# Optimization experiments

Measured on AMD Instinct MI355X. Metric: run time of the kernel, lower is better.

## Reference

```python
import jax, jax.numpy as jnp
import numpy as np

DIM = 1024
TOPK = 64
PAIRS = DIM // 2  # phase_pairs default
PHASE_MIX = 0.5
GATE_THRESHOLD = 0.0
EPS = 1e-12  # F.normalize default eps


def _l2norm(v):
    # matches F.normalize(v, dim=-1): v / max(||v||, eps)
    n = jnp.linalg.norm(v, axis=-1, keepdims=True)
    return v / jnp.maximum(n, EPS)


def setup_inputs() -> dict:
    key = jax.random.key(0)
    ks = jax.random.split(key, 6)
    s = 0.02  # small init scale for weights
    return {
        "x": jax.random.normal(ks[0], (4, 4096, DIM), dtype=jnp.float32),
        "gate_W": jax.random.normal(ks[1], (DIM, DIM), dtype=jnp.float32) * s,
        "gate_b": jnp.zeros((DIM,), dtype=jnp.float32),
        "mag_W": jax.random.normal(ks[2], (DIM, DIM), dtype=jnp.float32) * s,
        "mag_b": jnp.zeros((DIM,), dtype=jnp.float32),
        "Wq": jax.random.normal(ks[3], (DIM, DIM), dtype=jnp.float32) * s,
        "Wk": jax.random.normal(ks[4], (DIM, DIM), dtype=jnp.float32) * s,
        "phase_W": jax.random.normal(ks[5], (2 * PAIRS, DIM), dtype=jnp.float32) * s,
    }


def reference(x, gate_W, gate_b, mag_W, mag_b, Wq, Wk, phase_W):
    B, S, D = x.shape
    # gated SAE-style projection (gated=True, diag=False)
    gate_pre = x @ gate_W.T + gate_b          # [B,S,D]
    mag_pre = x @ mag_W.T + mag_b             # [B,S,D]
    # hard gate with straight-through estimator
    gate_soft = jax.nn.sigmoid(gate_pre)
    gate_hard = (gate_pre > GATE_THRESHOLD).astype(x.dtype)
    gate = gate_hard + gate_soft - jax.lax.stop_gradient(gate_soft)
    mag = jax.nn.relu(mag_pre)
    # top-k scatter mask along feature dim
    idx = jax.lax.top_k(gate_pre, TOPK)[1]    # [B,S,K]
    rows = jnp.arange(B * S)[:, None]
    mask = (jnp.zeros((B * S, D), dtype=bool)
            .at[rows, idx.reshape(B * S, TOPK)].set(True)
            .reshape(B, S, D))
    gate = jnp.where(mask, gate, jnp.zeros_like(gate))
    mag = jnp.where(mask, mag, jnp.zeros_like(mag))
    xg = gate * mag
    # twist projections, L2-normalized
    q = _l2norm(xg @ Wq.T)
    k = _l2norm(xg @ Wk.T)
    # symplectic momentum map over consecutive steps
    momentum_map = q[:, 1:] * k[:, :-1] - q[:, :-1] * k[:, 1:]  # [B,S-1,D]
    twist_mag = jnp.linalg.norm(momentum_map, axis=-1, keepdims=True)
    complexity = jnp.pad(jnp.tanh(twist_mag), ((0, 0), (1, 0), (0, 0)))  # [B,S,1]
    # phase branch (phase_mix > 0)
    phase = (xg @ phase_W.T).reshape(B, S, PAIRS, 2)
    phase = _l2norm(phase)
    pp, pc = phase[:, :-1], phase[:, 1:]
    cross = pp[..., 0] * pc[..., 1] - pp[..., 1] * pc[..., 0]   # [B,S-1,P]
    dot = jnp.clip(jnp.sum(pp * pc, axis=-1), -1.0, 1.0)
    phase_delta = jnp.abs(jnp.arctan2(cross, dot)) / jnp.pi
    phase_score = jnp.pad(jnp.mean(phase_delta, axis=-1, keepdims=True),
                          ((0, 0), (1, 0), (0, 0)))             # [B,S,1]
    return (1.0 - PHASE_MIX) * complexity + PHASE_MIX * phase_score
```

## Files before the change

### kernel.cpp

```cpp
#include <hip/hip_runtime.h>
#include <math.h>

#define DIM 1024
#define ROWS 16384
#define SEQ 4096
#define MARGIN 0.006f
#define MAXC 24

typedef __bf16 v8bf __attribute__((ext_vector_type(8)));
typedef float v4f __attribute__((ext_vector_type(4)));

__device__ __forceinline__ unsigned short f2bf(float f){
  unsigned u = __float_as_uint(f);
  u = u + 0x7FFFu + ((u >> 16) & 1u);
  return (unsigned short)(u >> 16);
}
__device__ __forceinline__ float bf2f(unsigned short h){
  return __uint_as_float(((unsigned)h) << 16);
}
__device__ __forceinline__ unsigned short relu_bf(unsigned short h){
  return (h & 0x8000u) ? (unsigned short)0 : h;
}
__device__ __forceinline__ void lds_fence(){
  __asm__ volatile("s_waitcnt lgkmcnt(0)" ::: "memory");
}

__global__ __launch_bounds__(256) void cvt_k(const float* __restrict__ s,
                                             unsigned short* __restrict__ d, int n){
  int i = (blockIdx.x * 256 + threadIdx.x) * 4;
  if (i + 3 < n){
    float4 f = *(const float4*)(s + i);
    ushort4 o;
    o.x = f2bf(f.x); o.y = f2bf(f.y); o.z = f2bf(f.z); o.w = f2bf(f.w);
    *(ushort4*)(d + i) = o;
  }
}

__global__ __launch_bounds__(256) void cvt_w(
    const float* __restrict__ w0, const float* __restrict__ w1,
    const float* __restrict__ w2, const float* __restrict__ w3,
    const float* __restrict__ w4, unsigned short* __restrict__ dst){
  const float* srcs[5] = {w0, w1, w2, w3, w4};
  const float* s = srcs[blockIdx.y];
  int i = (blockIdx.x * 256 + threadIdx.x) * 4;
  float4 f = *(const float4*)(s + i);
  ushort4 o;
  o.x = f2bf(f.x); o.y = f2bf(f.y); o.z = f2bf(f.z); o.w = f2bf(f.w);
  *(ushort4*)(dst + ((size_t)blockIdx.y << 20) + i) = o;
}

__global__ __launch_bounds__(256, 4) void gemm_bt(
    const unsigned short* __restrict__ A, const unsigned short* __restrict__ B,
    const float* __restrict__ bias0, const float* __restrict__ bias1,
    void* __restrict__ C0, void* __restrict__ C1, void* __restrict__ C2,
    int bf16mask)
{
  __shared__ unsigned short lA[128 * 32];
  __shared__ unsigned short lB[128 * 32];
  const int t = threadIdx.x;
  const int lane = t & 63, wave = t >> 6;
  const int m0 = blockIdx.y * 128, n0 = blockIdx.x * 128;
  const int wm = (wave >> 1) * 64, wn = (wave & 1) * 64;
  const int ar = lane & 15, aq = lane >> 4;

  v4f acc[4][4];
#pragma unroll
  for (int i = 0; i < 4; i++)
#pragma unroll
    for (int j = 0; j < 4; j++) acc[i][j] = v4f{0.f, 0.f, 0.f, 0.f};

  for (int k0 = 0; k0 < DIM; k0 += 32){
#pragma unroll
    for (int i = 0; i < 2; i++){
      int c = (wave * 2 + i) * 64 + lane;
      int row = c >> 2, kq = c & 3;
      __builtin_amdgcn_global_load_lds(
        (const __attribute__((address_space(1))) void*)(A + (size_t)(m0 + row) * DIM + k0 + kq * 8),
        (__attribute__((address_space(3))) void*)(&lA[c * 8]), 16, 0, 0);
      __builtin_amdgcn_global_load_lds(
        (const __attribute__((address_space(1))) void*)(B + (size_t)(n0 + row) * DIM + k0 + kq * 8),
        (__attribute__((address_space(3))) void*)(&lB[c * 8]), 16, 0, 0);
    }
    __syncthreads();
    v8bf af[4], bf[4];
#pragma unroll
    for (int i = 0; i < 4; i++){
      af[i] = *(const v8bf*)&lA[(wm + i * 16 + ar) * 32 + aq * 8];
      bf[i] = *(const v8bf*)&lB[(wn + i * 16 + ar) * 32 + aq * 8];
    }
#pragma unroll
    for (int mi = 0; mi < 4; mi++)
#pragma unroll
      for (int ni = 0; ni < 4; ni++)
        acc[mi][ni] = __builtin_amdgcn_mfma_f32_16x16x32_bf16(af[mi], bf[ni], acc[mi][ni], 0, 0, 0);
    __syncthreads();
  }

  const int os = n0 >> 10;
  void* Cp = (os == 0) ? C0 : ((os == 1) ? C1 : C2);
  const float* bp = (os == 0) ? bias0 : ((os == 1) ? bias1 : nullptr);
  const bool half_out = ((bf16mask >> os) & 1) != 0;
#pragma unroll
  for (int mi = 0; mi < 4; mi++)
#pragma unroll
    for (int ni = 0; ni < 4; ni++){
      int col = (n0 + wn + ni * 16 + ar) & (DIM - 1);
      float bv = bp ? bp[col] : 0.f;
#pragma unroll
      for (int rr = 0; rr < 4; rr++){
        int rowg = m0 + wm + mi * 16 + aq * 4 + rr;
        float val = acc[mi][ni][rr] + bv;
        if (half_out) ((unsigned short*)Cp)[(size_t)rowg * DIM + col] = f2bf(val);
        else          ((float*)Cp)[(size_t)rowg * DIM + col] = val;
      }
    }
}

__global__ __launch_bounds__(256) void select_k(
  const float* __restrict__ gate_pre, const unsigned short* __restrict__ mag_pre,
  const float* __restrict__ x, const float* __restrict__ gW, const float* __restrict__ gb,
  unsigned short* __restrict__ xg)
{
  __shared__ int   s_cnt[4];
  __shared__ int   s_idx[4][MAXC];
  __shared__ float s_ex [4][MAXC];
  __shared__ int   s_res[4][MAXC];

  const int t = threadIdx.x;
  const int lane = t & 63, wave = t >> 6;
  const int r = blockIdx.x * 4 + wave;
  const size_t rb = (size_t)r * DIM;

  float vg[16], vx[16];
  unsigned short mg[16];
#pragma unroll
  for (int c = 0; c < 4; c++){
    float4 g4 = *(const float4*)(gate_pre + rb + c * 256 + lane * 4);
    float4 x4 = *(const float4*)(x        + rb + c * 256 + lane * 4);
    ushort4 m4 = *(const ushort4*)(mag_pre + rb + c * 256 + lane * 4);
    vg[c*4+0]=g4.x; vg[c*4+1]=g4.y; vg[c*4+2]=g4.z; vg[c*4+3]=g4.w;
    vx[c*4+0]=x4.x; vx[c*4+1]=x4.y; vx[c*4+2]=x4.z; vx[c*4+3]=x4.w;
    mg[c*4+0]=m4.x; mg[c*4+1]=m4.y; mg[c*4+2]=m4.z; mg[c*4+3]=m4.w;
  }
  if (lane == 0) s_cnt[wave] = 0;

  float lo = -8.f, hi = 8.f;
#pragma unroll
  for (int it = 0; it < 15; it++){
    float mid = 0.5f * (lo + hi);
    int cn = 0;
#pragma unroll
    for (int e = 0; e < 16; e++) cn += (vg[e] > mid) ? 1 : 0;
#pragma unroll
    for (int m = 32; m; m >>= 1) cn += __shfl_xor(cn, m);
    if (cn >= 64) lo = mid; else hi = mid;
  }
  const float cl = lo - MARGIN, ch = hi + MARGIN;

  int n1 = 0;
#pragma unroll
  for (int e = 0; e < 16; e++) n1 += (vg[e] > ch) ? 1 : 0;
#pragma unroll
  for (int m = 32; m; m >>= 1) n1 += __shfl_xor(n1, m);
  const int s = 64 - n1;

  lds_fence();
#pragma unroll
  for (int e = 0; e < 16; e++){
    float vv = vg[e];
    if (vv >= cl && vv <= ch){
      int p = atomicAdd(&s_cnt[wave], 1);
      if (p < MAXC) s_idx[wave][p] = (e >> 2) * 256 + lane * 4 + (e & 3);
    }
  }
  lds_fence();
  int namb = s_cnt[wave]; if (namb > MAXC) namb = MAXC;

  for (int i = 0; i < namb; i++){
    int d = s_idx[wave][i];
    const float* wr = gW + (size_t)d * DIM;
    float p = 0.f;
#pragma unroll
    for (int c = 0; c < 4; c++){
      float4 w4 = *(const float4*)(wr + c * 256 + lane * 4);
      p = fmaf(vx[c*4+0], w4.x, p); p = fmaf(vx[c*4+1], w4.y, p);
      p = fmaf(vx[c*4+2], w4.z, p); p = fmaf(vx[c*4+3], w4.w, p);
    }
#pragma unroll
    for (int m = 32; m; m >>= 1) p += __shfl_xor(p, m);
    if (lane == 0) s_ex[wave][i] = p + gb[d];
  }
  lds_fence();

  if (lane < namb){
    float e = s_ex[wave][lane]; int d = s_idx[wave][lane];
    int rank = 0;
    for (int j = 0; j < namb; j++){
      float ej = s_ex[wave][j]; int dj = s_idx[wave][j];
      if (ej > e || (ej == e && dj < d)) rank++;
    }
    s_res[wave][lane] = (rank < s && e > 0.f) ? 1 : 0;
  }
  lds_fence();

  unsigned short o16[16];
#pragma unroll
  for (int e = 0; e < 16; e++)
    o16[e] = (vg[e] > ch) ? ((vg[e] > 0.f) ? relu_bf(mg[e]) : (unsigned short)0)
                          : (unsigned short)0;
  for (int i = 0; i < namb; i++){
    int d = s_idx[wave][i];
    int res = s_res[wave][i];
    if (((d >> 2) & 63) == lane){
      int e = (d >> 8) * 4 + (d & 3);
      o16[e] = res ? relu_bf(mg[e]) : (unsigned short)0;
    }
  }
#pragma unroll
  for (int c = 0; c < 4; c++){
    ushort4 o; o.x = o16[c*4+0]; o.y = o16[c*4+1]; o.z = o16[c*4+2]; o.w = o16[c*4+3];
    *(ushort4*)(xg + rb + c * 256 + lane * 4) = o;
  }
}

__global__ __launch_bounds__(256) void epilogue_k(
  const unsigned short* __restrict__ q_pre, const unsigned short* __restrict__ k_pre,
  const unsigned short* __restrict__ p_pre, float* __restrict__ out)
{
  const int r0 = blockIdx.x * 4;
  const int t = threadIdx.x;
  const int lane = t & 63, wave = t >> 6;
  __shared__ float red[16];

  const int rp = (r0 == 0) ? 0 : r0 - 1;
  float vqp[4], vkp[4], vpp[4];
  {
    ushort4 uq = *(const ushort4*)(q_pre + (size_t)rp * DIM + 4*t);
    ushort4 uk = *(const ushort4*)(k_pre + (size_t)rp * DIM + 4*t);
    ushort4 up = *(const ushort4*)(p_pre + (size_t)rp * DIM + 4*t);
    vqp[0]=bf2f(uq.x); vqp[1]=bf2f(uq.y); vqp[2]=bf2f(uq.z); vqp[3]=bf2f(uq.w);
    vkp[0]=bf2f(uk.x); vkp[1]=bf2f(uk.y); vkp[2]=bf2f(uk.z); vkp[3]=bf2f(uk.w);
    vpp[0]=bf2f(up.x); vpp[1]=bf2f(up.y); vpp[2]=bf2f(up.z); vpp[3]=bf2f(up.w);
  }
  float aq = 0.f, ak = 0.f;
#pragma unroll
  for (int j = 0; j < 4; j++){ aq = fmaf(vqp[j], vqp[j], aq); ak = fmaf(vkp[j], vkp[j], ak); }
#pragma unroll
  for (int m = 32; m; m >>= 1){ aq += __shfl_xor(aq, m); ak += __shfl_xor(ak, m); }
  if (lane == 0){ red[wave] = aq; red[4 + wave] = ak; }
  __syncthreads();
  float rqp = 1.f / fmaxf(sqrtf(red[0] + red[1] + red[2] + red[3]), 1e-12f);
  float rkp = 1.f / fmaxf(sqrtf(red[4] + red[5] + red[6] + red[7]), 1e-12f);
  __syncthreads();

  for (int rr = 0; rr < 4; rr++){
    const int r = r0 + rr;
    float vqc[4], vkc[4], vpc[4];
    {
      ushort4 uq = *(const ushort4*)(q_pre + (size_t)r * DIM + 4*t);
      ushort4 uk = *(const ushort4*)(k_pre + (size_t)r * DIM + 4*t);
      ushort4 up = *(const ushort4*)(p_pre + (size_t)r * DIM + 4*t);
      vqc[0]=bf2f(uq.x); vqc[1]=bf2f(uq.y); vqc[2]=bf2f(uq.z); vqc[3]=bf2f(uq.w);
      vkc[0]=bf2f(uk.x); vkc[1]=bf2f(uk.y); vkc[2]=bf2f(uk.z); vkc[3]=bf2f(uk.w);
      vpc[0]=bf2f(up.x); vpc[1]=bf2f(up.y); vpc[2]=bf2f(up.z); vpc[3]=bf2f(up.w);
    }
    const bool seg = (r & (SEQ - 1)) == 0;
    float aqc = 0.f, akc = 0.f;
#pragma unroll
    for (int j = 0; j < 4; j++){ aqc = fmaf(vqc[j], vqc[j], aqc); akc = fmaf(vkc[j], vkc[j], akc); }
    float dsum = 0.f;
    if (!seg){
#pragma unroll
      for (int j = 0; j < 2; j++){
        float ax = vpp[2*j], ay = vpp[2*j+1], bx = vpc[2*j], by = vpc[2*j+1];
        float ia = 1.f / fmaxf(sqrtf(ax * ax + ay * ay), 1e-12f);
        float ib = 1.f / fmaxf(sqrtf(bx * bx + by * by), 1e-12f);
        ax *= ia; ay *= ia; bx *= ib; by *= ib;
        float cross = ax * by - ay * bx;
        float dot = fminf(fmaxf(ax * bx + ay * by, -1.f), 1.f);
        dsum += fabsf(atan2f(cross, dot)) * 0.3183098861837907f;
      }
    }
#pragma unroll
    for (int m = 32; m; m >>= 1){
      aqc += __shfl_xor(aqc, m); akc += __shfl_xor(akc, m); dsum += __shfl_xor(dsum, m);
    }
    if (lane == 0){ red[wave] = aqc; red[4 + wave] = akc; red[8 + wave] = dsum; }
    __syncthreads();
    float rqc = 1.f / fmaxf(sqrtf(red[0] + red[1] + red[2] + red[3]), 1e-12f);
    float rkc = 1.f / fmaxf(sqrtf(red[4] + red[5] + red[6] + red[7]), 1e-12f);
    if (!seg){
      float tw = 0.f;
#pragma unroll
      for (int j = 0; j < 4; j++){
        float m = (vqc[j] * rqc) * (vkp[j] * rkp) - (vqp[j] * rqp) * (vkc[j] * rkc);
        tw = fmaf(m, m, tw);
      }
#pragma unroll
      for (int m = 32; m; m >>= 1) tw += __shfl_xor(tw, m);
      if (lane == 0) red[12 + wave] = tw;
      __syncthreads();
      if (t == 0){
        float dtot = red[8] + red[9] + red[10] + red[11];
        float twt = red[12] + red[13] + red[14] + red[15];
        out[r] = 0.5f * tanhf(sqrtf(twt)) + 0.5f * (dtot * (1.f / 512.f));
      }
    } else {
      if (t == 0) out[r] = 0.f;
    }
    __syncthreads();
#pragma unroll
    for (int j = 0; j < 4; j++){ vqp[j] = vqc[j]; vkp[j] = vkc[j]; vpp[j] = vpc[j]; }
    rqp = rqc; rkp = rkc;
  }
}

extern "C" void kernel_launch(void* const* d_in, const int* in_sizes, int n_in,
                              void* d_out, int out_size, void* d_ws, size_t ws_size,
                              hipStream_t stream)
{
  const float* x       = (const float*)d_in[0];
  const float* gate_W  = (const float*)d_in[1];
  const float* gate_b  = (const float*)d_in[2];
  const float* mag_W   = (const float*)d_in[3];
  const float* mag_b   = (const float*)d_in[4];
  const float* Wq      = (const float*)d_in[5];
  const float* Wk      = (const float*)d_in[6];
  const float* phase_W = (const float*)d_in[7];
  float* out = (float*)d_out;

  char* ws = (char*)d_ws;
  unsigned short* xbf = (unsigned short*)ws;
  unsigned short* wbf = (unsigned short*)(ws + 33554432);
  float*          gate_pre = (float*)(ws + 46137344);
  unsigned short* mag_pre  = (unsigned short*)(ws + 113246208);
  unsigned short* p_pre    = (unsigned short*)(ws + 146800640);
  unsigned short* q_pre = (unsigned short*)gate_pre;
  unsigned short* k_pre = mag_pre;

  dim3 b256(256);
  cvt_k<<<16384, b256, 0, stream>>>(x, xbf, ROWS * DIM);
  cvt_w<<<dim3(1024, 5), b256, 0, stream>>>(gate_W, mag_W, Wq, Wk, phase_W, wbf);

  gemm_bt<<<dim3(16, 128), b256, 0, stream>>>(xbf, wbf, gate_b, mag_b,
                                              gate_pre, mag_pre, nullptr, 0b010);

  unsigned short* xg = xbf;
  select_k<<<ROWS / 4, b256, 0, stream>>>(gate_pre, mag_pre, x, gate_W, gate_b, xg);

  gemm_bt<<<dim3(24, 128), b256, 0, stream>>>(xg, wbf + (2u << 20), nullptr, nullptr,
                                              q_pre, k_pre, p_pre, 0b111);

  epilogue_k<<<ROWS / 4, b256, 0, stream>>>(q_pre, k_pre, p_pre, out);
}
```

Measured before the change: 422.1 us.

## Store gate_pre in bf16, merge conversion kernels, and remap GEMM block order

gate_pre is now written by the first GEMM in bf16 instead of fp32, which halves its write and read traffic. The top-k candidate margin is widened to absorb the extra rounding error, with exact recomputation left to the unchanged fallback path. The x and weight conversion kernels are merged into one launch. GEMM blocks are now ordered M-fastest, so consecutive blocks share the same B tile, which should improve L2 reuse. The risk is more boundary candidates, possibly overflowing MAXC, which would cost more recompute or give wrong selections.

```diff
diff --git a/kernel.cpp b/kernel.cpp
--- a/kernel.cpp
+++ b/kernel.cpp
@@ -4,7 +4,7 @@
 #define DIM 1024
 #define ROWS 16384
 #define SEQ 4096
-#define MARGIN 0.006f
+#define MARGIN 0.012f
 #define MAXC 24
 
 typedef __bf16 v8bf __attribute__((ext_vector_type(8)));
@@ -25,28 +25,25 @@
   __asm__ volatile("s_waitcnt lgkmcnt(0)" ::: "memory");
 }
 
-__global__ __launch_bounds__(256) void cvt_k(const float* __restrict__ s,
-                                             unsigned short* __restrict__ d, int n){
-  int i = (blockIdx.x * 256 + threadIdx.x) * 4;
-  if (i + 3 < n){
-    float4 f = *(const float4*)(s + i);
-    ushort4 o;
-    o.x = f2bf(f.x); o.y = f2bf(f.y); o.z = f2bf(f.z); o.w = f2bf(f.w);
-    *(ushort4*)(d + i) = o;
-  }
-}
-
-__global__ __launch_bounds__(256) void cvt_w(
+__global__ __launch_bounds__(256) void cvt_all(
+    const float* __restrict__ x,
     const float* __restrict__ w0, const float* __restrict__ w1,
     const float* __restrict__ w2, const float* __restrict__ w3,
-    const float* __restrict__ w4, unsigned short* __restrict__ dst){
-  const float* srcs[5] = {w0, w1, w2, w3, w4};
-  const float* s = srcs[blockIdx.y];
+    const float* __restrict__ w4,
+    unsigned short* __restrict__ xbf, unsigned short* __restrict__ wbf){
+  const int y = blockIdx.y;
+  const float* s;
+  unsigned short* d;
+  if (y < 16){ s = x + ((size_t)y << 20); d = xbf + ((size_t)y << 20); }
+  else {
+    const float* srcs[5] = {w0, w1, w2, w3, w4};
+    s = srcs[y - 16]; d = wbf + ((size_t)(y - 16) << 20);
+  }
   int i = (blockIdx.x * 256 + threadIdx.x) * 4;
   float4 f = *(const float4*)(s + i);
   ushort4 o;
   o.x = f2bf(f.x); o.y = f2bf(f.y); o.z = f2bf(f.z); o.w = f2bf(f.w);
-  *(ushort4*)(dst + ((size_t)blockIdx.y << 20) + i) = o;
+  *(ushort4*)(d + i) = o;
 }
 
 __global__ __launch_bounds__(256, 4) void gemm_bt(
@@ -59,7 +56,9 @@
   __shared__ unsigned short lB[128 * 32];
   const int t = threadIdx.x;
   const int lane = t & 63, wave = t >> 6;
-  const int m0 = blockIdx.y * 128, n0 = blockIdx.x * 128;
+  const int bid = blockIdx.y * gridDim.x + blockIdx.x;
+  const int m0 = (bid & 127) * 128;
+  const int n0 = (bid >> 7) * 128;
   const int wm = (wave >> 1) * 64, wn = (wave & 1) * 64;
   const int ar = lane & 15, aq = lane >> 4;
 
@@ -117,7 +116,7 @@
 }
 
 __global__ __launch_bounds__(256) void select_k(
-  const float* __restrict__ gate_pre, const unsigned short* __restrict__ mag_pre,
+  const unsigned short* __restrict__ gate_pre, const unsigned short* __restrict__ mag_pre,
   const float* __restrict__ x, const float* __restrict__ gW, const float* __restrict__ gb,
   unsigned short* __restrict__ xg)
 {
@@ -135,10 +134,10 @@
   unsigned short mg[16];
 #pragma unroll
   for (int c = 0; c < 4; c++){
-    float4 g4 = *(const float4*)(gate_pre + rb + c * 256 + lane * 4);
-    float4 x4 = *(const float4*)(x        + rb + c * 256 + lane * 4);
-    ushort4 m4 = *(const ushort4*)(mag_pre + rb + c * 256 + lane * 4);
-    vg[c*4+0]=g4.x; vg[c*4+1]=g4.y; vg[c*4+2]=g4.z; vg[c*4+3]=g4.w;
+    ushort4 g4 = *(const ushort4*)(gate_pre + rb + c * 256 + lane * 4);
+    float4 x4 = *(const float4*)(x          + rb + c * 256 + lane * 4);
+    ushort4 m4 = *(const ushort4*)(mag_pre  + rb + c * 256 + lane * 4);
+    vg[c*4+0]=bf2f(g4.x); vg[c*4+1]=bf2f(g4.y); vg[c*4+2]=bf2f(g4.z); vg[c*4+3]=bf2f(g4.w);
     vx[c*4+0]=x4.x; vx[c*4+1]=x4.y; vx[c*4+2]=x4.z; vx[c*4+3]=x4.w;
     mg[c*4+0]=m4.x; mg[c*4+1]=m4.y; mg[c*4+2]=m4.z; mg[c*4+3]=m4.w;
   }
@@ -332,18 +331,17 @@
   char* ws = (char*)d_ws;
   unsigned short* xbf = (unsigned short*)ws;
   unsigned short* wbf = (unsigned short*)(ws + 33554432);
-  float*          gate_pre = (float*)(ws + 46137344);
-  unsigned short* mag_pre  = (unsigned short*)(ws + 113246208);
-  unsigned short* p_pre    = (unsigned short*)(ws + 146800640);
-  unsigned short* q_pre = (unsigned short*)gate_pre;
+  unsigned short* gate_pre = (unsigned short*)(ws + 46137344);
+  unsigned short* mag_pre  = (unsigned short*)(ws + 79691776);
+  unsigned short* p_pre    = (unsigned short*)(ws + 113246208);
+  unsigned short* q_pre = gate_pre;
   unsigned short* k_pre = mag_pre;
 
   dim3 b256(256);
-  cvt_k<<<16384, b256, 0, stream>>>(x, xbf, ROWS * DIM);
-  cvt_w<<<dim3(1024, 5), b256, 0, stream>>>(gate_W, mag_W, Wq, Wk, phase_W, wbf);
+  cvt_all<<<dim3(1024, 21), b256, 0, stream>>>(x, gate_W, mag_W, Wq, Wk, phase_W, xbf, wbf);
 
   gemm_bt<<<dim3(16, 128), b256, 0, stream>>>(xbf, wbf, gate_b, mag_b,
-                                              gate_pre, mag_pre, nullptr, 0b010);
+                                              gate_pre, mag_pre, nullptr, 0b011);
 
   unsigned short* xg = xbf;
   select_k<<<ROWS / 4, b256, 0, stream>>>(gate_pre, mag_pre, x, gate_W, gate_b, xg);
```

New measurement: 425.1 us. About the same (+0.7%).
